# Kernel tuning notes

Measured on AMD Instinct MI355X. Metric: run time of the kernel, lower is better.

The kernel has to match this reference:

```python
import jax, jax.numpy as jnp
import numpy as np

D_MODEL = 128
NEG_INF = -1e30


def setup_inputs() -> dict:
    key = jax.random.key(0)
    k1, k2, k3, k4 = jax.random.split(key, 4)
    B, Lc, Lq, d = 32, 2048, 256, D_MODEL
    C = jax.random.normal(k1, (B, Lc, d), dtype=jnp.float32)
    Q = jax.random.normal(k2, (B, Lq, d), dtype=jnp.float32)
    # Linear(3d, 1): weight laid out for cat order (Q_, C_, C_*Q_)
    w = jax.random.normal(k3, (3 * d,), dtype=jnp.float32) / np.sqrt(3 * d)
    b = jax.random.normal(k4, (1,), dtype=jnp.float32) * 0.01
    c_mask = jnp.ones((B, Lc), dtype=jnp.int32)
    q_mask = jnp.ones((B, Lq), dtype=jnp.int32)
    return {"C": C, "Q": Q, "w": w, "b": b, "c_mask": c_mask, "q_mask": q_mask}


def reference(C, Q, w, b, c_mask, q_mask):
    d = C.shape[-1]
    # Algebraic decomposition of Linear([Q_, C_, C_*Q_]) -> scalar:
    # S[b,i,j] = Q[b,j]@w_q + C[b,i]@w_c + (C[b,i]*w_m)@Q[b,j] + bias
    w_q, w_c, w_m = w[:d], w[d:2 * d], w[2 * d:]
    S = (C @ w_c)[:, :, None] \
        + (Q @ w_q)[:, None, :] \
        + jnp.einsum('bid,bjd->bij', C * w_m, Q) \
        + b[0]                                        # (B, Lc, Lq)
    mask = (c_mask[:, :, None] * q_mask[:, None, :]).astype(S.dtype)
    S = S * mask + NEG_INF * (1.0 - mask)
    S1 = jax.nn.softmax(S, axis=1)  # softmax over context dim (as in source)
    S2 = jax.nn.softmax(S, axis=2)  # softmax over query dim
    C2Q = jnp.einsum('bij,bjd->bid', S1, Q)           # (B, Lc, d)
    # Q2C = S1 @ S2^T @ C, associated as S1 @ (S2^T @ C) to avoid (Lc,Lc)
    T = jnp.einsum('bkj,bkd->bjd', S2, C)             # (B, Lq, d)
    Q2C = jnp.einsum('bij,bjd->bid', S1, T)           # (B, Lc, d)
    out = jnp.concatenate([C, C2Q, C * C2Q, C * Q2C], axis=2)  # (B, Lc, 4d)
    # dropout omitted (deterministic reference / eval mode)
    return out
```

## Files before the change

### kernel.cpp

```cpp
#include <hip/hip_runtime.h>


#define LC 2048
#define LQ 256
#define DM 128
#define NEG_INF_F (-1e30f)

using bf16x8  = __attribute__((ext_vector_type(8))) __bf16;
using f32x4   = __attribute__((ext_vector_type(4))) float;
using ushort8 = __attribute__((ext_vector_type(8))) unsigned short;

__device__ __forceinline__ unsigned short f2bf(float x) {
    unsigned int u = __float_as_uint(x);
    u += 0x7fffu + ((u >> 16) & 1u);
    return (unsigned short)(u >> 16);
}
__device__ __forceinline__ float bf2f(unsigned short h) {
    return __uint_as_float(((unsigned int)h) << 16);
}
__device__ __forceinline__ f32x4 mfma16(bf16x8 a, bf16x8 b, f32x4 c) {
    return __builtin_amdgcn_mfma_f32_16x16x32_bf16(a, b, c, 0, 0, 0);
}

__global__ __launch_bounds__(256) void k_preQ(const float* __restrict__ Q,
        const float* __restrict__ w, unsigned short* __restrict__ Qbf,
        unsigned short* __restrict__ Qt, float* __restrict__ rq) {
    const int b = blockIdx.z, j0 = blockIdx.x * 64, d0 = blockIdx.y * 64;
    const int tid = threadIdx.x;
    __shared__ float tile[64][65];
    __shared__ float wq[128];
    if (tid < 128) wq[tid] = w[tid];
    __syncthreads();
    const int r = tid >> 2, c0 = (tid & 3) * 16;
    const float4* sp = (const float4*)(Q + (size_t)(b * LQ + j0 + r) * DM + d0 + c0);
    float v[16];
#pragma unroll
    for (int u = 0; u < 4; ++u) {
        float4 t = sp[u];
        v[4*u] = t.x; v[4*u+1] = t.y; v[4*u+2] = t.z; v[4*u+3] = t.w;
    }
    unsigned short ob[16];
    float p = 0.f;
#pragma unroll
    for (int u = 0; u < 16; ++u) {
        ob[u] = f2bf(v[u]);
        p += v[u] * wq[d0 + c0 + u];
        tile[r][c0 + u] = v[u];
    }
    ushort8* qb = (ushort8*)(Qbf + (size_t)(b * LQ + j0 + r) * DM + d0 + c0);
    qb[0] = *(ushort8*)&ob[0];
    qb[1] = *(ushort8*)&ob[8];
    p += __shfl_xor(p, 1);
    p += __shfl_xor(p, 2);
    if ((tid & 3) == 0) atomicAdd(&rq[b * LQ + j0 + r], p);
    __syncthreads();
    unsigned short o[16];
#pragma unroll
    for (int u = 0; u < 16; ++u) o[u] = f2bf(tile[c0 + u][r]);
    ushort8* dp = (ushort8*)(Qt + (size_t)(b * DM + d0 + r) * LQ + j0 + c0);
    dp[0] = *(ushort8*)&o[0];
    dp[1] = *(ushort8*)&o[8];
}

__global__ __launch_bounds__(256) void k_preC(const float* __restrict__ C,
        unsigned short* __restrict__ Ct) {
    const int b = blockIdx.z, i0 = blockIdx.x * 64, d0 = blockIdx.y * 64;
    const int tid = threadIdx.x;
    __shared__ float tile[64][65];
    const int r = tid >> 2, c0 = (tid & 3) * 16;
    const float4* sp = (const float4*)(C + (size_t)(b * LC + i0 + r) * DM + d0 + c0);
#pragma unroll
    for (int u = 0; u < 4; ++u) {
        float4 t = sp[u];
        tile[r][c0 + 4*u] = t.x; tile[r][c0 + 4*u + 1] = t.y;
        tile[r][c0 + 4*u + 2] = t.z; tile[r][c0 + 4*u + 3] = t.w;
    }
    __syncthreads();
    unsigned short o[16];
#pragma unroll
    for (int u = 0; u < 16; ++u) o[u] = f2bf(tile[c0 + u][r]);
    ushort8* dp = (ushort8*)(Ct + (size_t)(b * DM + d0 + r) * LC + i0 + c0);
    dp[0] = *(ushort8*)&o[0];
    dp[1] = *(ushort8*)&o[8];
}

__global__ __launch_bounds__(256) void k1_scores(
    const float* __restrict__ C, const unsigned short* __restrict__ Qbf,
    const float* __restrict__ w, const float* __restrict__ bptr,
    const int* __restrict__ c_mask, const int* __restrict__ q_mask,
    const float* __restrict__ rq,
    unsigned short* __restrict__ E, float* __restrict__ l1g, float* __restrict__ l2g) {
    const int b = blockIdx.y;
    const int i0 = blockIdx.x * 64;
    const int tid = threadIdx.x;
    const int lane = tid & 63, wid = tid >> 6;
    const int quad = lane >> 4, l15 = lane & 15;

    __shared__ unsigned short Alds[64][136];
    __shared__ float wsm[256];
    __shared__ float rcs[64], rqs[256], cms[64], qms[256], l2s[64];
    __shared__ float b0s;

    if (tid < 256) {
        wsm[tid] = w[128 + tid];
        rqs[tid] = rq[b * LQ + tid];
        qms[tid] = (float)q_mask[b * LQ + tid];
    }
    if (tid < 64) {
        cms[tid] = (float)c_mask[b * LC + i0 + tid];
        l2s[tid] = 0.f;
    }
    if (tid == 0) b0s = bptr[0];
    __syncthreads();

    {
        const int r = tid >> 2, qq = tid & 3;
        const float4* cp = (const float4*)(C + (size_t)(b * LC + i0 + r) * DM + qq * 32);
        float prc = 0.f;
#pragma unroll
        for (int u = 0; u < 8; ++u) {
            float4 v = cp[u];
            const int c0 = qq * 32 + u * 4;
            prc += v.x * wsm[c0] + v.y * wsm[c0 + 1] + v.z * wsm[c0 + 2] + v.w * wsm[c0 + 3];
            Alds[r][c0 + 0] = f2bf(v.x * wsm[128 + c0]);
            Alds[r][c0 + 1] = f2bf(v.y * wsm[129 + c0]);
            Alds[r][c0 + 2] = f2bf(v.z * wsm[130 + c0]);
            Alds[r][c0 + 3] = f2bf(v.w * wsm[131 + c0]);
        }
        prc += __shfl_xor(prc, 1);
        prc += __shfl_xor(prc, 2);
        if (qq == 0) rcs[r] = prc;
    }
    __syncthreads();

    const int n_base = wid * 64;
    const unsigned short* qbase = Qbf + (size_t)b * LQ * DM;
    const f32x4 z4 = {0.f, 0.f, 0.f, 0.f};
    f32x4 acc[4][4];
#pragma unroll
    for (int mt = 0; mt < 4; ++mt)
#pragma unroll
        for (int nt = 0; nt < 4; ++nt) acc[mt][nt] = z4;

#pragma unroll
    for (int kc = 0; kc < 4; ++kc) {
        const int ko = kc * 32 + quad * 8;
        bf16x8 af[4], bfr[4];
#pragma unroll
        for (int mt = 0; mt < 4; ++mt)
            af[mt] = *(const bf16x8*)&Alds[mt * 16 + l15][ko];
#pragma unroll
        for (int nt = 0; nt < 4; ++nt)
            bfr[nt] = *(const bf16x8*)(qbase + (size_t)(n_base + nt * 16 + l15) * DM + ko);
#pragma unroll
        for (int mt = 0; mt < 4; ++mt)
#pragma unroll
            for (int nt = 0; nt < 4; ++nt)
                acc[mt][nt] = mfma16(af[mt], bfr[nt], acc[mt][nt]);
    }

    const float b0 = b0s;
    float colsum[4] = {0.f, 0.f, 0.f, 0.f};
#pragma unroll
    for (int mt = 0; mt < 4; ++mt) {
#pragma unroll
        for (int reg = 0; reg < 4; ++reg) {
            const int m = mt * 16 + quad * 4 + reg;
            float rowsum = 0.f;
#pragma unroll
            for (int nt = 0; nt < 4; ++nt) {
                const int n = n_base + nt * 16 + l15;
                float s = acc[mt][nt][reg] + rcs[m] + rqs[n] + b0;
                const float mk = cms[m] * qms[n];
                s = s * mk + NEG_INF_F * (1.f - mk);
                const float e = __expf(s);
                acc[mt][nt][reg] = e;
                rowsum += e;
                colsum[nt] += e;
            }
            rowsum += __shfl_xor(rowsum, 1);
            rowsum += __shfl_xor(rowsum, 2);
            rowsum += __shfl_xor(rowsum, 4);
            rowsum += __shfl_xor(rowsum, 8);
            if (l15 == 0) atomicAdd(&l2s[m], rowsum);
        }
    }
#pragma unroll
    for (int nt = 0; nt < 4; ++nt) {
        float v = colsum[nt];
        v += __shfl_xor(v, 16);
        v += __shfl_xor(v, 32);
        if (quad == 0) atomicAdd(&l1g[b * LQ + n_base + nt * 16 + l15], v);
    }
    __syncthreads();
    if (tid < 64) l2g[b * LC + i0 + tid] = l2s[tid];

#pragma unroll
    for (int mt = 0; mt < 4; ++mt) {
#pragma unroll
        for (int reg = 0; reg < 4; ++reg) {
            const int m = mt * 16 + quad * 4 + reg;
            const float rl = 1.0f / l2s[m];
            unsigned short* erow = E + (size_t)(b * LC + i0 + m) * LQ;
#pragma unroll
            for (int nt = 0; nt < 4; ++nt) {
                const int n = n_base + nt * 16 + l15;
                erow[n] = f2bf(acc[mt][nt][reg] * rl);
            }
        }
    }
}

__global__ __launch_bounds__(256) void kS_scaleQt(
    const unsigned short* __restrict__ Qt, const float* __restrict__ l1g,
    unsigned short* __restrict__ Qts) {
    const int b = blockIdx.y;
    const int tid = threadIdx.x;
    __shared__ float rl1s[256];
    rl1s[tid] = 1.0f / l1g[b * LQ + tid];
    __syncthreads();
    const int idx = blockIdx.x * 256 + tid;
    const int d = idx >> 5, jc = (idx & 31) * 8;
    const ushort8 v = *(const ushort8*)(Qt + (size_t)(b * DM + d) * LQ + jc);
    unsigned short o[8];
#pragma unroll
    for (int u = 0; u < 8; ++u) o[u] = f2bf(bf2f(v[u]) * rl1s[jc + u]);
    *(ushort8*)(Qts + (size_t)(b * DM + d) * LQ + jc) = *(ushort8*)&o[0];
}

__global__ __launch_bounds__(512) void k3_Tt(
    const unsigned short* __restrict__ E, const unsigned short* __restrict__ Ct,
    const float* __restrict__ l1g, unsigned short* __restrict__ Tt) {
    const int j0 = blockIdx.x * 64, d0 = blockIdx.y * 64, b = blockIdx.z;
    const int tid = threadIdx.x;
    const int lane = tid & 63, wid = tid >> 6;
    const int quad = lane >> 4, l15 = lane & 15;
    const int m_base = (wid >> 1) * 16, n32 = (wid & 1) * 32;

    __shared__ unsigned short Ab[64][136];
    __shared__ unsigned short Bb[64][136];
    __shared__ float rl1s[64];
    if (tid < 64) rl1s[tid] = 1.0f / l1g[b * LQ + j0 + tid];

    const f32x4 z4 = {0.f, 0.f, 0.f, 0.f};
    f32x4 acc[2] = {z4, z4};

    for (int it = 0; it < 16; ++it) {
        const int ic = it * 128;
        __syncthreads();
        {
            const int r = tid >> 3, q = tid & 7;
            const ushort8* cp = (const ushort8*)(Ct + (size_t)(b * DM + d0 + r) * LC + ic + q * 16);
            *(ushort8*)&Ab[r][q * 16] = cp[0];
            *(ushort8*)&Ab[r][q * 16 + 8] = cp[1];
        }
        {
            const int il = tid >> 2, sg = (tid & 3) * 16;
            const ushort8* ep = (const ushort8*)(E + (size_t)(b * LC + ic + il) * LQ + j0 + sg);
            ushort8 e0 = ep[0], e1 = ep[1];
#pragma unroll
            for (int u = 0; u < 8; ++u) Bb[sg + u][il] = e0[u];
#pragma unroll
            for (int u = 0; u < 8; ++u) Bb[sg + 8 + u][il] = e1[u];
        }
        __syncthreads();
#pragma unroll
        for (int kk = 0; kk < 4; ++kk) {
            const int ko = kk * 32 + quad * 8;
            bf16x8 af = *(const bf16x8*)&Ab[m_base + l15][ko];
            bf16x8 b0f = *(const bf16x8*)&Bb[n32 + l15][ko];
            bf16x8 b1f = *(const bf16x8*)&Bb[n32 + 16 + l15][ko];
            acc[0] = mfma16(af, b0f, acc[0]);
            acc[1] = mfma16(af, b1f, acc[1]);
        }
    }
#pragma unroll
    for (int nt = 0; nt < 2; ++nt)
#pragma unroll
        for (int reg = 0; reg < 4; ++reg) {
            const int dd = d0 + m_base + quad * 4 + reg;
            const int jl = n32 + nt * 16 + l15;
            Tt[(size_t)(b * DM + dd) * LQ + j0 + jl] = f2bf(acc[nt][reg] * rl1s[jl]);
        }
}

__global__ __launch_bounds__(256) void k4_out(
    const unsigned short* __restrict__ E, const float* __restrict__ C,
    const unsigned short* __restrict__ Qts, const unsigned short* __restrict__ Tt,
    const float* __restrict__ l2g, float* __restrict__ out) {
    const int b = blockIdx.y;
    const int i0 = blockIdx.x * 64;
    const int tid = threadIdx.x;
    const int lane = tid & 63, wid = tid >> 6;
    const int quad = lane >> 4, l15 = lane & 15;
    const int n_base = wid * 32;

    __shared__ unsigned short Aq[64][72];
    __shared__ unsigned short Bq[128][72];
    __shared__ unsigned short Bt2[128][72];
    __shared__ float l2s[64];
    if (tid < 64) l2s[tid] = l2g[b * LC + i0 + tid];

    const f32x4 z4 = {0.f, 0.f, 0.f, 0.f};
    f32x4 acc1[4][2], acc2[4][2];
#pragma unroll
    for (int mt = 0; mt < 4; ++mt)
#pragma unroll
        for (int nt = 0; nt < 2; ++nt) { acc1[mt][nt] = z4; acc2[mt][nt] = z4; }

#pragma unroll 1
    for (int kc = 0; kc < 4; ++kc) {
        const int jc = kc * 64;
        __syncthreads();
        {
            const int r = tid >> 2, q = tid & 3;
            const ushort8* ep = (const ushort8*)(E + (size_t)(b * LC + i0 + r) * LQ + jc + q * 16);
            *(ushort8*)&Aq[r][q * 16] = ep[0];
            *(ushort8*)&Aq[r][q * 16 + 8] = ep[1];
        }
        {
            const int r = tid >> 1, h = (tid & 1) * 32;
            const ushort8* qp = (const ushort8*)(Qts + (size_t)(b * DM + r) * LQ + jc + h);
            const ushort8* tp = (const ushort8*)(Tt + (size_t)(b * DM + r) * LQ + jc + h);
#pragma unroll
            for (int u = 0; u < 4; ++u) {
                *(ushort8*)&Bq[r][h + u * 8] = qp[u];
                *(ushort8*)&Bt2[r][h + u * 8] = tp[u];
            }
        }
        __syncthreads();
#pragma unroll
        for (int kk = 0; kk < 2; ++kk) {
            const int ko = kk * 32 + quad * 8;
            bf16x8 a[4], bq[2], bt[2];
#pragma unroll
            for (int mt = 0; mt < 4; ++mt)
                a[mt] = *(const bf16x8*)&Aq[mt * 16 + l15][ko];
#pragma unroll
            for (int nt = 0; nt < 2; ++nt) {
                bq[nt] = *(const bf16x8*)&Bq[n_base + nt * 16 + l15][ko];
                bt[nt] = *(const bf16x8*)&Bt2[n_base + nt * 16 + l15][ko];
            }
#pragma unroll
            for (int mt = 0; mt < 4; ++mt)
#pragma unroll
                for (int nt = 0; nt < 2; ++nt) {
                    acc1[mt][nt] = mfma16(a[mt], bq[nt], acc1[mt][nt]);
                    acc2[mt][nt] = mfma16(a[mt], bt[nt], acc2[mt][nt]);
                }
        }
    }

#pragma unroll
    for (int mt = 0; mt < 4; ++mt)
#pragma unroll
        for (int reg = 0; reg < 4; ++reg) {
            const int il = mt * 16 + quad * 4 + reg;
            const int i = i0 + il;
            const float l2v = l2s[il];
            const size_t rb = (size_t)(b * LC + i) * 512;
            const float* crow = C + (size_t)(b * LC + i) * DM;
#pragma unroll
            for (int nt = 0; nt < 2; ++nt) {
                const int d = n_base + nt * 16 + l15;
                const float c = crow[d];
                const float v1 = acc1[mt][nt][reg] * l2v;
                const float v2 = acc2[mt][nt][reg] * l2v;
                out[rb + d] = c;
                out[rb + 128 + d] = v1;
                out[rb + 256 + d] = c * v1;
                out[rb + 384 + d] = c * v2;
            }
        }
}

extern "C" void kernel_launch(void* const* d_in, const int* in_sizes, int n_in,
                              void* d_out, int out_size, void* d_ws, size_t ws_size,
                              hipStream_t stream) {
    const float* C = (const float*)d_in[0];
    const float* Q = (const float*)d_in[1];
    const float* w = (const float*)d_in[2];
    const float* bp = (const float*)d_in[3];
    const int* cm = (const int*)d_in[4];
    const int* qm = (const int*)d_in[5];
    float* out = (float*)d_out;

    char* ws = (char*)d_ws;
    unsigned short* E   = (unsigned short*)(ws);
    unsigned short* Ct  = (unsigned short*)(ws + 33554432);
    unsigned short* Qbf = (unsigned short*)(ws + 50331648);
    unsigned short* Qt  = (unsigned short*)(ws + 52428800);
    unsigned short* Qts = (unsigned short*)(ws + 54525952);
    unsigned short* Tt  = (unsigned short*)(ws + 56623104);
    float*          l2g = (float*)(ws + 58720256);
    float*          rq  = (float*)(ws + 58982400);
    float*          l1  = (float*)(ws + 59015168);

    hipMemsetAsync(ws + 58982400, 0, 65536, stream);

    k_preQ<<<dim3(4, 2, 32), 256, 0, stream>>>(Q, w, Qbf, Qt, rq);
    k_preC<<<dim3(32, 2, 32), 256, 0, stream>>>(C, Ct);
    k1_scores<<<dim3(32, 32), 256, 0, stream>>>(C, Qbf, w, bp, cm, qm, rq, E, l1, l2g);
    kS_scaleQt<<<dim3(16, 32), 256, 0, stream>>>(Qt, l1, Qts);
    k3_Tt<<<dim3(4, 2, 32), 512, 0, stream>>>(E, Ct, l1, Tt);
    k4_out<<<dim3(32, 32), 256, 0, stream>>>(E, C, Qts, Tt, l2g, out);
}
```

Before: 257.0 us.

## Write transposed E from scores kernel, fuse prep kernels, fold l1 scaling into out kernel

The scores kernel now stages its normalized E tile in LDS and also writes a transposed copy ET. This lets the T kernel load both operands with vectorized row loads instead of doing a scalar LDS transpose, and it now uses 256 threads with a 2x2 MFMA tile per wave. The Q and C prep kernels are merged into one launch. The separate Qt-scaling kernel is removed by applying 1/l1 to E tiles inside the output kernel, which also drops the l1 division in the T kernel. The cost is an extra 32MB of ET writes and reads and more per-element conversion work in the output kernel.

Result: slower. 267.1 us (+3.9%).

```diff
diff --git a/kernel.cpp b/kernel.cpp
--- a/kernel.cpp
+++ b/kernel.cpp
@@ -22,66 +22,66 @@
     return __builtin_amdgcn_mfma_f32_16x16x32_bf16(a, b, c, 0, 0, 0);
 }
 
-__global__ __launch_bounds__(256) void k_preQ(const float* __restrict__ Q,
-        const float* __restrict__ w, unsigned short* __restrict__ Qbf,
-        unsigned short* __restrict__ Qt, float* __restrict__ rq) {
-    const int b = blockIdx.z, j0 = blockIdx.x * 64, d0 = blockIdx.y * 64;
+__global__ __launch_bounds__(256) void k_prep(const float* __restrict__ Q,
+        const float* __restrict__ C, const float* __restrict__ w,
+        unsigned short* __restrict__ Qbf, unsigned short* __restrict__ Qt,
+        unsigned short* __restrict__ Ct, float* __restrict__ rq) {
+    const int b = blockIdx.z, bx = blockIdx.x;
     const int tid = threadIdx.x;
     __shared__ float tile[64][65];
     __shared__ float wq[128];
-    if (tid < 128) wq[tid] = w[tid];
-    __syncthreads();
     const int r = tid >> 2, c0 = (tid & 3) * 16;
-    const float4* sp = (const float4*)(Q + (size_t)(b * LQ + j0 + r) * DM + d0 + c0);
-    float v[16];
-#pragma unroll
-    for (int u = 0; u < 4; ++u) {
-        float4 t = sp[u];
-        v[4*u] = t.x; v[4*u+1] = t.y; v[4*u+2] = t.z; v[4*u+3] = t.w;
-    }
-    unsigned short ob[16];
-    float p = 0.f;
-#pragma unroll
-    for (int u = 0; u < 16; ++u) {
-        ob[u] = f2bf(v[u]);
-        p += v[u] * wq[d0 + c0 + u];
-        tile[r][c0 + u] = v[u];
-    }
-    ushort8* qb = (ushort8*)(Qbf + (size_t)(b * LQ + j0 + r) * DM + d0 + c0);
-    qb[0] = *(ushort8*)&ob[0];
-    qb[1] = *(ushort8*)&ob[8];
-    p += __shfl_xor(p, 1);
-    p += __shfl_xor(p, 2);
-    if ((tid & 3) == 0) atomicAdd(&rq[b * LQ + j0 + r], p);
-    __syncthreads();
-    unsigned short o[16];
-#pragma unroll
-    for (int u = 0; u < 16; ++u) o[u] = f2bf(tile[c0 + u][r]);
-    ushort8* dp = (ushort8*)(Qt + (size_t)(b * DM + d0 + r) * LQ + j0 + c0);
-    dp[0] = *(ushort8*)&o[0];
-    dp[1] = *(ushort8*)&o[8];
-}
-
-__global__ __launch_bounds__(256) void k_preC(const float* __restrict__ C,
-        unsigned short* __restrict__ Ct) {
-    const int b = blockIdx.z, i0 = blockIdx.x * 64, d0 = blockIdx.y * 64;
-    const int tid = threadIdx.x;
-    __shared__ float tile[64][65];
-    const int r = tid >> 2, c0 = (tid & 3) * 16;
-    const float4* sp = (const float4*)(C + (size_t)(b * LC + i0 + r) * DM + d0 + c0);
-#pragma unroll
-    for (int u = 0; u < 4; ++u) {
-        float4 t = sp[u];
-        tile[r][c0 + 4*u] = t.x; tile[r][c0 + 4*u + 1] = t.y;
-        tile[r][c0 + 4*u + 2] = t.z; tile[r][c0 + 4*u + 3] = t.w;
-    }
-    __syncthreads();
-    unsigned short o[16];
-#pragma unroll
-    for (int u = 0; u < 16; ++u) o[u] = f2bf(tile[c0 + u][r]);
-    ushort8* dp = (ushort8*)(Ct + (size_t)(b * DM + d0 + r) * LC + i0 + c0);
-    dp[0] = *(ushort8*)&o[0];
-    dp[1] = *(ushort8*)&o[8];
+
+    if (bx < 8) {
+        const int j0 = (bx & 3) * 64, d0 = (bx >> 2) * 64;
+        if (tid < 128) wq[tid] = w[tid];
+        __syncthreads();
+        const float4* sp = (const float4*)(Q + (size_t)(b * LQ + j0 + r) * DM + d0 + c0);
+        float v[16];
+#pragma unroll
+        for (int u = 0; u < 4; ++u) {
+            float4 t = sp[u];
+            v[4*u] = t.x; v[4*u+1] = t.y; v[4*u+2] = t.z; v[4*u+3] = t.w;
+        }
+        unsigned short ob[16];
+        float p = 0.f;
+#pragma unroll
+        for (int u = 0; u < 16; ++u) {
+            ob[u] = f2bf(v[u]);
+            p += v[u] * wq[d0 + c0 + u];
+            tile[r][c0 + u] = v[u];
+        }
+        ushort8* qb = (ushort8*)(Qbf + (size_t)(b * LQ + j0 + r) * DM + d0 + c0);
+        qb[0] = *(ushort8*)&ob[0];
+        qb[1] = *(ushort8*)&ob[8];
+        p += __shfl_xor(p, 1);
+        p += __shfl_xor(p, 2);
+        if ((tid & 3) == 0) atomicAdd(&rq[b * LQ + j0 + r], p);
+        __syncthreads();
+        unsigned short o[16];
+#pragma unroll
+        for (int u = 0; u < 16; ++u) o[u] = f2bf(tile[c0 + u][r]);
+        ushort8* dp = (ushort8*)(Qt + (size_t)(b * DM + d0 + r) * LQ + j0 + c0);
+        dp[0] = *(ushort8*)&o[0];
+        dp[1] = *(ushort8*)&o[8];
+    } else {
+        const int x = bx - 8;
+        const int i0 = (x >> 1) * 64, d0 = (x & 1) * 64;
+        const float4* sp = (const float4*)(C + (size_t)(b * LC + i0 + r) * DM + d0 + c0);
+#pragma unroll
+        for (int u = 0; u < 4; ++u) {
+            float4 t = sp[u];
+            tile[r][c0 + 4*u] = t.x; tile[r][c0 + 4*u + 1] = t.y;
+            tile[r][c0 + 4*u + 2] = t.z; tile[r][c0 + 4*u + 3] = t.w;
+        }
+        __syncthreads();
+        unsigned short o[16];
+#pragma unroll
+        for (int u = 0; u < 16; ++u) o[u] = f2bf(tile[c0 + u][r]);
+        ushort8* dp = (ushort8*)(Ct + (size_t)(b * DM + d0 + r) * LC + i0 + c0);
+        dp[0] = *(ushort8*)&o[0];
+        dp[1] = *(ushort8*)&o[8];
+    }
 }
 
 __global__ __launch_bounds__(256) void k1_scores(
@@ -89,14 +89,16 @@
     const float* __restrict__ w, const float* __restrict__ bptr,
     const int* __restrict__ c_mask, const int* __restrict__ q_mask,
     const float* __restrict__ rq,
-    unsigned short* __restrict__ E, float* __restrict__ l1g, float* __restrict__ l2g) {
+    unsigned short* __restrict__ E, unsigned short* __restrict__ ET,
+    float* __restrict__ l1g, float* __restrict__ l2g) {
     const int b = blockIdx.y;
     const int i0 = blockIdx.x * 64;
     const int tid = threadIdx.x;
     const int lane = tid & 63, wid = tid >> 6;
     const int quad = lane >> 4, l15 = lane & 15;
 
-    __shared__ unsigned short Alds[64][136];
+    __shared__ unsigned short ETl[256][72];
+    unsigned short (*Alds)[136] = (unsigned short (*)[136])&ETl[0][0];
     __shared__ float wsm[256];
     __shared__ float rcs[64], rqs[256], cms[64], qms[256], l2s[64];
     __shared__ float b0s;
@@ -205,89 +207,84 @@
 #pragma unroll
             for (int nt = 0; nt < 4; ++nt) {
                 const int n = n_base + nt * 16 + l15;
-                erow[n] = f2bf(acc[mt][nt][reg] * rl);
-            }
-        }
-    }
-}
-
-__global__ __launch_bounds__(256) void kS_scaleQt(
-    const unsigned short* __restrict__ Qt, const float* __restrict__ l1g,
-    unsigned short* __restrict__ Qts) {
-    const int b = blockIdx.y;
-    const int tid = threadIdx.x;
-    __shared__ float rl1s[256];
-    rl1s[tid] = 1.0f / l1g[b * LQ + tid];
+                const unsigned short ev = f2bf(acc[mt][nt][reg] * rl);
+                erow[n] = ev;
+                ETl[n][m] = ev;
+            }
+        }
+    }
     __syncthreads();
-    const int idx = blockIdx.x * 256 + tid;
-    const int d = idx >> 5, jc = (idx & 31) * 8;
-    const ushort8 v = *(const ushort8*)(Qt + (size_t)(b * DM + d) * LQ + jc);
-    unsigned short o[8];
-#pragma unroll
-    for (int u = 0; u < 8; ++u) o[u] = f2bf(bf2f(v[u]) * rl1s[jc + u]);
-    *(ushort8*)(Qts + (size_t)(b * DM + d) * LQ + jc) = *(ushort8*)&o[0];
-}
-
-__global__ __launch_bounds__(512) void k3_Tt(
-    const unsigned short* __restrict__ E, const unsigned short* __restrict__ Ct,
-    const float* __restrict__ l1g, unsigned short* __restrict__ Tt) {
+
+    const int jr = tid >> 1, h = tid & 1;
+#pragma unroll
+    for (int rr = 0; rr < 2; ++rr) {
+        const int j = jr + rr * 128;
+        const unsigned short* lp = &ETl[j][h * 32];
+        ushort8* gp = (ushort8*)(ET + (size_t)(b * LQ + j) * LC + i0 + h * 32);
+#pragma unroll
+        for (int u = 0; u < 4; ++u) gp[u] = *(const ushort8*)(lp + u * 8);
+    }
+}
+
+__global__ __launch_bounds__(256) void k3_Tt(
+    const unsigned short* __restrict__ ET, const unsigned short* __restrict__ Ct,
+    unsigned short* __restrict__ Tt) {
     const int j0 = blockIdx.x * 64, d0 = blockIdx.y * 64, b = blockIdx.z;
     const int tid = threadIdx.x;
     const int lane = tid & 63, wid = tid >> 6;
     const int quad = lane >> 4, l15 = lane & 15;
-    const int m_base = (wid >> 1) * 16, n32 = (wid & 1) * 32;
+    const int m32 = (wid & 1) * 32, n32 = (wid >> 1) * 32;
 
     __shared__ unsigned short Ab[64][136];
     __shared__ unsigned short Bb[64][136];
-    __shared__ float rl1s[64];
-    if (tid < 64) rl1s[tid] = 1.0f / l1g[b * LQ + j0 + tid];
 
     const f32x4 z4 = {0.f, 0.f, 0.f, 0.f};
-    f32x4 acc[2] = {z4, z4};
-
+    f32x4 acc[2][2] = {{z4, z4}, {z4, z4}};
+
+    const int r = tid >> 2, q = tid & 3;
     for (int it = 0; it < 16; ++it) {
         const int ic = it * 128;
         __syncthreads();
         {
-            const int r = tid >> 3, q = tid & 7;
-            const ushort8* cp = (const ushort8*)(Ct + (size_t)(b * DM + d0 + r) * LC + ic + q * 16);
-            *(ushort8*)&Ab[r][q * 16] = cp[0];
-            *(ushort8*)&Ab[r][q * 16 + 8] = cp[1];
-        }
-        {
-            const int il = tid >> 2, sg = (tid & 3) * 16;
-            const ushort8* ep = (const ushort8*)(E + (size_t)(b * LC + ic + il) * LQ + j0 + sg);
-            ushort8 e0 = ep[0], e1 = ep[1];
-#pragma unroll
-            for (int u = 0; u < 8; ++u) Bb[sg + u][il] = e0[u];
-#pragma unroll
-            for (int u = 0; u < 8; ++u) Bb[sg + 8 + u][il] = e1[u];
+            const ushort8* cp = (const ushort8*)(Ct + (size_t)(b * DM + d0 + r) * LC + ic + q * 32);
+            const ushort8* ep = (const ushort8*)(ET + (size_t)(b * LQ + j0 + r) * LC + ic + q * 32);
+#pragma unroll
+            for (int u = 0; u < 4; ++u) {
+                *(ushort8*)&Ab[r][q * 32 + u * 8] = cp[u];
+                *(ushort8*)&Bb[r][q * 32 + u * 8] = ep[u];
+            }
         }
         __syncthreads();
 #pragma unroll
         for (int kk = 0; kk < 4; ++kk) {
             const int ko = kk * 32 + quad * 8;
-            bf16x8 af = *(const bf16x8*)&Ab[m_base + l15][ko];
-            bf16x8 b0f = *(const bf16x8*)&Bb[n32 + l15][ko];
-            bf16x8 b1f = *(const bf16x8*)&Bb[n32 + 16 + l15][ko];
-            acc[0] = mfma16(af, b0f, acc[0]);
-            acc[1] = mfma16(af, b1f, acc[1]);
-        }
-    }
-#pragma unroll
-    for (int nt = 0; nt < 2; ++nt)
-#pragma unroll
-        for (int reg = 0; reg < 4; ++reg) {
-            const int dd = d0 + m_base + quad * 4 + reg;
-            const int jl = n32 + nt * 16 + l15;
-            Tt[(size_t)(b * DM + dd) * LQ + j0 + jl] = f2bf(acc[nt][reg] * rl1s[jl]);
-        }
+            bf16x8 a0 = *(const bf16x8*)&Ab[m32 + l15][ko];
+            bf16x8 a1 = *(const bf16x8*)&Ab[m32 + 16 + l15][ko];
+            bf16x8 b0 = *(const bf16x8*)&Bb[n32 + l15][ko];
+            bf16x8 b1 = *(const bf16x8*)&Bb[n32 + 16 + l15][ko];
+            acc[0][0] = mfma16(a0, b0, acc[0][0]);
+            acc[0][1] = mfma16(a0, b1, acc[0][1]);
+            acc[1][0] = mfma16(a1, b0, acc[1][0]);
+            acc[1][1] = mfma16(a1, b1, acc[1][1]);
+        }
+    }
+#pragma unroll
+    for (int mt = 0; mt < 2; ++mt)
+#pragma unroll
+        for (int nt = 0; nt < 2; ++nt)
+#pragma unroll
+            for (int reg = 0; reg < 4; ++reg) {
+                const int d = d0 + m32 + mt * 16 + quad * 4 + reg;
+                const int j = j0 + n32 + nt * 16 + l15;
+                Tt[(size_t)(b * DM + d) * LQ + j] = f2bf(acc[mt][nt][reg]);
+            }
 }
 
 __global__ __launch_bounds__(256) void k4_out(
     const unsigned short* __restrict__ E, const float* __restrict__ C,
-    const unsigned short* __restrict__ Qts, const unsigned short* __restrict__ Tt,
-    const float* __restrict__ l2g, float* __restrict__ out) {
+    const unsigned short* __restrict__ Qt, const unsigned short* __restrict__ Tt,
+    const float* __restrict__ l1g, const float* __restrict__ l2g,
+    float* __restrict__ out) {
     const int b = blockIdx.y;
     const int i0 = blockIdx.x * 64;
     const int tid = threadIdx.x;
@@ -298,8 +295,10 @@
     __shared__ unsigned short Aq[64][72];
     __shared__ unsigned short Bq[128][72];
     __shared__ unsigned short Bt2[128][72];
-    __shared__ float l2s[64];
-    if (tid < 64) l2s[tid] = l2g[b * LC + i0 + tid];
+    __shared__ float rl1s[256];
+    __shared__ float l2sm[64];
+    rl1s[tid] = 1.0f / l1g[b * LQ + tid];
+    if (tid < 64) l2sm[tid] = l2g[b * LC + i0 + tid];
 
     const f32x4 z4 = {0.f, 0.f, 0.f, 0.f};
     f32x4 acc1[4][2], acc2[4][2];
@@ -315,12 +314,19 @@
         {
             const int r = tid >> 2, q = tid & 3;
             const ushort8* ep = (const ushort8*)(E + (size_t)(b * LC + i0 + r) * LQ + jc + q * 16);
-            *(ushort8*)&Aq[r][q * 16] = ep[0];
-            *(ushort8*)&Aq[r][q * 16 + 8] = ep[1];
+            ushort8 e0 = ep[0], e1 = ep[1];
+            unsigned short o0[8], o1[8];
+#pragma unroll
+            for (int u = 0; u < 8; ++u) {
+                o0[u] = f2bf(bf2f(e0[u]) * rl1s[jc + q * 16 + u]);
+                o1[u] = f2bf(bf2f(e1[u]) * rl1s[jc + q * 16 + 8 + u]);
+            }
+            *(ushort8*)&Aq[r][q * 16] = *(ushort8*)&o0[0];
+            *(ushort8*)&Aq[r][q * 16 + 8] = *(ushort8*)&o1[0];
         }
         {
             const int r = tid >> 1, h = (tid & 1) * 32;
-            const ushort8* qp = (const ushort8*)(Qts + (size_t)(b * DM + r) * LQ + jc + h);
+            const ushort8* qp = (const ushort8*)(Qt + (size_t)(b * DM + r) * LQ + jc + h);
             const ushort8* tp = (const ushort8*)(Tt + (size_t)(b * DM + r) * LQ + jc + h);
 #pragma unroll
             for (int u = 0; u < 4; ++u) {
@@ -357,7 +363,7 @@
         for (int reg = 0; reg < 4; ++reg) {
             const int il = mt * 16 + quad * 4 + reg;
             const int i = i0 + il;
-            const float l2v = l2s[il];
+            const float l2v = l2sm[il];
             const size_t rb = (size_t)(b * LC + i) * 512;
             const float* crow = C + (size_t)(b * LC + i) * DM;
 #pragma unroll
@@ -387,21 +393,19 @@
 
     char* ws = (char*)d_ws;
     unsigned short* E   = (unsigned short*)(ws);
-    unsigned short* Ct  = (unsigned short*)(ws + 33554432);
-    unsigned short* Qbf = (unsigned short*)(ws + 50331648);
-    unsigned short* Qt  = (unsigned short*)(ws + 52428800);
-    unsigned short* Qts = (unsigned short*)(ws + 54525952);
-    unsigned short* Tt  = (unsigned short*)(ws + 56623104);
-    float*          l2g = (float*)(ws + 58720256);
-    float*          rq  = (float*)(ws + 58982400);
-    float*          l1  = (float*)(ws + 59015168);
-
-    hipMemsetAsync(ws + 58982400, 0, 65536, stream);
-
-    k_preQ<<<dim3(4, 2, 32), 256, 0, stream>>>(Q, w, Qbf, Qt, rq);
-    k_preC<<<dim3(32, 2, 32), 256, 0, stream>>>(C, Ct);
-    k1_scores<<<dim3(32, 32), 256, 0, stream>>>(C, Qbf, w, bp, cm, qm, rq, E, l1, l2g);
-    kS_scaleQt<<<dim3(16, 32), 256, 0, stream>>>(Qt, l1, Qts);
-    k3_Tt<<<dim3(4, 2, 32), 512, 0, stream>>>(E, Ct, l1, Tt);
-    k4_out<<<dim3(32, 32), 256, 0, stream>>>(E, C, Qts, Tt, l2g, out);
-}
+    unsigned short* ET  = (unsigned short*)(ws + 33554432);
+    unsigned short* Ct  = (unsigned short*)(ws + 67108864);
+    unsigned short* Qbf = (unsigned short*)(ws + 83886080);
+    unsigned short* Qt  = (unsigned short*)(ws + 85983232);
+    unsigned short* Tt  = (unsigned short*)(ws + 88080384);
+    float*          l2g = (float*)(ws + 90177536);
+    float*          rq  = (float*)(ws + 90439680);
+    float*          l1  = (float*)(ws + 90472448);
+
+    hipMemsetAsync(ws + 90439680, 0, 65536, stream);
+
+    k_prep<<<dim3(72, 1, 32), 256, 0, stream>>>(Q, C, w, Qbf, Qt, Ct, rq);
+    k1_scores<<<dim3(32, 32), 256, 0, stream>>>(C, Qbf, w, bp, cm, qm, rq, E, ET, l1, l2g);
+    k3_Tt<<<dim3(4, 2, 32), 256, 0, stream>>>(ET, Ct, Tt);
+    k4_out<<<dim3(32, 32), 256, 0, stream>>>(E, C, Qt, Tt, l1, l2g, out);
+}
```
